# Kernel tuning notes

Hardware: AMD Instinct MI355X
Metric: run time of the kernel (lower is better)

Reference implementation:

```python
import jax, jax.numpy as jnp
import numpy as np
from jax import lax

K = 3        # kernel size
PAD = 1      # padding
K2 = K * K


def conv2d(x, w, b):
    # x: [B,C,H,W], w: [O,C,K,K], b: [O]
    y = lax.conv_general_dilated(
        x, w, window_strides=(1, 1), padding=((PAD, PAD), (PAD, PAD)),
        dimension_numbers=("NCHW", "OIHW", "NCHW"))
    return y + b[None, :, None, None]


def bilinear_sample(img, py, px):
    # img: [C,H,W]; py, px: [K2,H,W] float sampling coords (zero padding outside)
    H, W = img.shape[1], img.shape[2]
    y0 = jnp.floor(py); x0 = jnp.floor(px)
    wy1 = py - y0; wx1 = px - x0
    wy0 = 1.0 - wy1; wx0 = 1.0 - wx1

    def gather(yi, xi, wgt):
        yc = jnp.clip(yi, 0, H - 1).astype(jnp.int32)
        xc = jnp.clip(xi, 0, W - 1).astype(jnp.int32)
        valid = ((yi >= 0) & (yi <= H - 1) & (xi >= 0) & (xi <= W - 1))
        v = img[:, yc, xc]                      # [C,K2,H,W]
        return v * (wgt * valid.astype(img.dtype))[None]

    return (gather(y0, x0, wy0 * wx0) + gather(y0, x0 + 1, wy0 * wx1)
            + gather(y0 + 1, x0, wy1 * wx0) + gather(y0 + 1, x0 + 1, wy1 * wx1))


def deform_conv2d(x, offset, weight, bias):
    # x: [B,C,H,W], offset: [B,2*K2,H,W] as (dy,dx) pairs per kernel tap
    B, C, H, W = x.shape
    off = offset.reshape(B, K2, 2, H, W)
    ks_y = (jnp.arange(K2) // K - PAD).astype(x.dtype)   # kernel tap y offsets
    ks_x = (jnp.arange(K2) % K - PAD).astype(x.dtype)
    base_y = ks_y[:, None, None] + jnp.arange(H, dtype=x.dtype)[None, :, None]
    base_x = ks_x[:, None, None] + jnp.arange(W, dtype=x.dtype)[None, None, :]
    py = off[:, :, 0] + base_y                            # [B,K2,H,W]
    px = off[:, :, 1] + base_x
    sampled = jax.vmap(bilinear_sample)(x, py, px)        # [B,C,K2,H,W]
    out = jnp.einsum("bckhw,ock->bohw", sampled, weight.reshape(weight.shape[0], C, K2))
    return out + bias[None, :, None, None]


def setup_inputs() -> dict:
    key = jax.random.key(0)
    ks = jax.random.split(key, 5)
    B, C, O, H, W = 4, 64, 64, 128, 128
    s_off = 1.0 / np.sqrt(C * K2)
    return {
        "x": jax.random.normal(ks[0], (B, C, H, W), dtype=jnp.float32),
        "w_off": jax.random.normal(ks[1], (2 * K2, C, K, K), dtype=jnp.float32) * s_off,
        "b_off": jnp.zeros((2 * K2,), dtype=jnp.float32),
        "weight": jax.random.normal(ks[2], (O, C, K, K), dtype=jnp.float32) * s_off,
        "bias": jax.random.normal(ks[3], (O,), dtype=jnp.float32) * 0.01,
    }


def reference(x, w_off, b_off, weight, bias):
    offset = conv2d(x, w_off, b_off)          # [B,18,H,W]
    return deform_conv2d(x, offset, weight, bias)
```

## Files before the change

kernel.cpp:

```cpp
#include <hip/hip_runtime.h>
#include <hip/hip_bf16.h>

#define BB 4
#define CC 64
#define OO 64
#define HH 128
#define WW 128
#define HW (HH * WW)
#define K2 9
#define OCOFF 18
#define SMP_STRIDE 36

typedef __attribute__((ext_vector_type(8))) short short8;
typedef __attribute__((ext_vector_type(16))) float f32x16;

union U8 { unsigned u[4]; short8 s8; };

__device__ __forceinline__ float uf(unsigned u) { return __builtin_bit_cast(float, u); }

__device__ __forceinline__ unsigned cvtpk(float a, float b) {
  unsigned r;
  asm("v_cvt_pk_bf16_f32 %0, %1, %2" : "=v"(r) : "v"(a), "v"(b));
  return r;
}
__device__ __forceinline__ void split2(float a, float b, unsigned& ph, unsigned& pl) {
  ph = cvtpk(a, b);
  float ra = a - uf(ph << 16);
  float rb = b - uf(ph & 0xFFFF0000u);
  pl = cvtpk(ra, rb);
}

__device__ __forceinline__ unsigned short bf16_rne(float v) {
  unsigned u = __builtin_bit_cast(unsigned, v);
  return (unsigned short)((u + 0x7FFFu + ((u >> 16) & 1u)) >> 16);
}
__device__ __forceinline__ void bf16_split(float v, unsigned short& hi, unsigned short& lo) {
  hi = bf16_rne(v);
  float hf = __builtin_bit_cast(float, (unsigned)hi << 16);
  lo = bf16_rne(v - hf);
}
__device__ __forceinline__ float4 ld4(const float* p) { return *(const float4*)p; }

__global__ __launch_bounds__(256) void prep_all(
    const float* __restrict__ x, const float* __restrict__ weight,
    const float* __restrict__ w_off, float* __restrict__ xt,
    unsigned* __restrict__ wf, unsigned* __restrict__ wof) {
  int blk = blockIdx.x;
  int t = threadIdx.x;
  if (blk < 2048) {
    __shared__ float tile[64][33];
    int wt = blk & 3, h = (blk >> 2) & 127, b = blk >> 9;
    int w0 = wt * 32;
    {
      int w_l = t & 31, c_l = t >> 5;
#pragma unroll
      for (int i = 0; i < 8; ++i) {
        int cc = c_l * 8 + i;
        tile[cc][w_l] = x[(((size_t)b * 64 + cc) * 128 + h) * 128 + w0 + w_l];
      }
    }
    __syncthreads();
    {
      int c_w = t & 63, w_w = t >> 6;
#pragma unroll
      for (int i = 0; i < 8; ++i) {
        int wl = w_w * 8 + i;
        xt[(((size_t)b * 128 + h) * 128 + w0 + wl) * 64 + c_w] = tile[c_w][wl];
      }
    }
    return;
  }
  if (blk < 2048 + 144) {
    int d = (blk - 2048) * 256 + t;
    if (d >= 9 * 4096) return;
    int j2 = d & 3, l = (d >> 2) & 63, hh = (d >> 8) & 1, s = (d >> 9) & 3,
        m = (d >> 11) & 1, c = d >> 12;
    int o = m * 32 + (l & 31);
    int g = l >> 5;
    int ch0 = s * 16 + g * 8 + j2 * 2;
    float v0 = weight[(o * 64 + ch0) * 9 + c];
    float v1 = weight[(o * 64 + ch0 + 1) * 9 + c];
    unsigned short h0, l0, h1, l1;
    bf16_split(v0, h0, l0);
    bf16_split(v1, h1, l1);
    unsigned short b0 = hh ? l0 : h0;
    unsigned short b1 = hh ? l1 : h1;
    wf[d] = (unsigned)b0 | ((unsigned)b1 << 16);
    return;
  }
  {
    int d = (blk - 2192) * 256 + t;
    if (d >= 9 * 2048) return;
    int j2 = d & 3, l = (d >> 2) & 63, hh = (d >> 8) & 1, s = (d >> 9) & 3,
        c = d >> 11;
    int oc = l & 31;
    int g = l >> 5;
    int ch0 = s * 16 + g * 8 + j2 * 2;
    unsigned r = 0;
    if (oc < OCOFF) {
      float v0 = w_off[(oc * 64 + ch0) * 9 + c];
      float v1 = w_off[(oc * 64 + ch0 + 1) * 9 + c];
      unsigned short h0, l0, h1, l1;
      bf16_split(v0, h0, l0);
      bf16_split(v1, h1, l1);
      unsigned short b0 = hh ? l0 : h0;
      unsigned short b1 = hh ? l1 : h1;
      r = (unsigned)b0 | ((unsigned)b1 << 16);
    }
    wof[d] = r;
    return;
  }
}

struct TapD { int o00, o01, o10, o11; float w00, w01, w10, w11; };
struct TapW { float w00, w01, w10, w11; };

__device__ __forceinline__ TapD mk_tapd(float oyv, float oxv, int h, int wpix, int kk) {
  TapD t;
  const int dy = kk / 3 - 1, dx = kk - (kk / 3) * 3 - 1;
  float py = oyv + (float)(h + dy);
  float px = oxv + (float)(wpix + dx);
  float y0f = floorf(py), x0f = floorf(px);
  float wy1 = py - y0f, wx1 = px - x0f;
  float wy0 = 1.0f - wy1, wx0 = 1.0f - wx1;
  int y0 = (int)y0f, x0 = (int)x0f, y1 = y0 + 1, x1 = x0 + 1;
  bool vy0 = (unsigned)y0 < (unsigned)HH, vy1 = (unsigned)y1 < (unsigned)HH;
  bool vx0 = (unsigned)x0 < (unsigned)WW, vx1 = (unsigned)x1 < (unsigned)WW;
  t.w00 = (vy0 && vx0) ? wy0 * wx0 : 0.0f;
  t.w01 = (vy0 && vx1) ? wy0 * wx1 : 0.0f;
  t.w10 = (vy1 && vx0) ? wy1 * wx0 : 0.0f;
  t.w11 = (vy1 && vx1) ? wy1 * wx1 : 0.0f;
  int y0c = min(max(y0, 0), HH - 1), y1c = min(max(y1, 0), HH - 1);
  int x0c = min(max(x0, 0), WW - 1), x1c = min(max(x1, 0), WW - 1);
  t.o00 = (y0c * WW + x0c) * CC;
  t.o01 = (y0c * WW + x1c) * CC;
  t.o10 = (y1c * WW + x0c) * CC;
  t.o11 = (y1c * WW + x1c) * CC;
  return t;
}

__device__ __forceinline__ TapW stageD2(float4 (&st)[8], const float* xb,
                                        const float* ol, int h, int wbase,
                                        int pq, int j4, int r, int c) {
  float2 o = *(const float2*)&ol[(r * 8 + pq) * OCOFF + 2 * c];
  TapD t = mk_tapd(o.x, o.y, h, wbase + r * 8 + pq, c);
  st[0] = ld4(xb + t.o00 + j4);      st[1] = ld4(xb + t.o01 + j4);
  st[2] = ld4(xb + t.o10 + j4);      st[3] = ld4(xb + t.o11 + j4);
  st[4] = ld4(xb + t.o00 + 32 + j4); st[5] = ld4(xb + t.o01 + 32 + j4);
  st[6] = ld4(xb + t.o10 + 32 + j4); st[7] = ld4(xb + t.o11 + 32 + j4);
  TapW w = { t.w00, t.w01, t.w10, t.w11 };
  return w;
}

__device__ __forceinline__ void consD(unsigned* mh, unsigned* ml,
                                      int pl, int j,
                                      const float4 (&st)[8], const TapW& t) {
#pragma unroll
  for (int hf = 0; hf < 2; ++hf) {
    float v[4];
#pragma unroll
    for (int q = 0; q < 4; ++q)
      v[q] = fmaf(t.w00, st[hf * 4 + 0][q], fmaf(t.w01, st[hf * 4 + 1][q],
             fmaf(t.w10, st[hf * 4 + 2][q], t.w11 * st[hf * 4 + 3][q])));
    unsigned h01, l01, h23, l23;
    split2(v[0], v[1], h01, l01);
    split2(v[2], v[3], h23, l23);
    int idx = pl * SMP_STRIDE + hf * 16 + j * 2;
    *(uint2*)&mh[idx] = make_uint2(h01, h23);
    *(uint2*)&ml[idx] = make_uint2(l01, l23);
  }
}

__device__ __forceinline__ void p2_mfma(f32x16& acc0, f32x16& acc1,
                                        const unsigned* mh, const unsigned* ml,
                                        const unsigned* wfrag,
                                        int P, int g, int l, int c) {
  __builtin_amdgcn_s_setprio(1);
#pragma unroll
  for (int s = 0; s < 4; ++s) {
    int ridx = P * SMP_STRIDE + s * 8 + g * 4;
    short8 sh8 = *(const short8*)&mh[ridx];
    short8 sl8 = *(const short8*)&ml[ridx];
    const unsigned* wb = wfrag + ((size_t)((c * 16 + s * 2) * 64 + l)) * 4;
    short8 wh0 = *(const short8*)(wb);
    short8 wl0 = *(const short8*)(wb + 256);
    short8 wh1 = *(const short8*)(wb + 2048);
    short8 wl1 = *(const short8*)(wb + 2304);
    acc0 = __builtin_amdgcn_mfma_f32_32x32x16_bf16(wh0, sh8, acc0, 0, 0, 0);
    acc0 = __builtin_amdgcn_mfma_f32_32x32x16_bf16(wh0, sl8, acc0, 0, 0, 0);
    acc0 = __builtin_amdgcn_mfma_f32_32x32x16_bf16(wl0, sh8, acc0, 0, 0, 0);
    acc1 = __builtin_amdgcn_mfma_f32_32x32x16_bf16(wh1, sh8, acc1, 0, 0, 0);
    acc1 = __builtin_amdgcn_mfma_f32_32x32x16_bf16(wh1, sl8, acc1, 0, 0, 0);
    acc1 = __builtin_amdgcn_mfma_f32_32x32x16_bf16(wl1, sh8, acc1, 0, 0, 0);
  }
  __builtin_amdgcn_s_setprio(0);
}

__device__ __forceinline__ unsigned stageO1(uint4 (&T)[8], const float* xb,
                                            int h, int wP, int g, int c) {
  const int dy = c / 3 - 1, dx = c - (c / 3) * 3 - 1;
  const int y = h + dy, xp = wP + dx;
  bool valid = ((unsigned)y < (unsigned)HH) && ((unsigned)xp < (unsigned)WW);
  int yc = min(max(y, 0), HH - 1), xc = min(max(xp, 0), WW - 1);
  const uint4* rowp = (const uint4*)(xb + (size_t)(yc * WW + xc) * CC);
#pragma unroll
  for (int s = 0; s < 4; ++s) {
    T[2 * s]     = rowp[s * 4 + g * 2];
    T[2 * s + 1] = rowp[s * 4 + g * 2 + 1];
  }
  return valid ? 0xFFFFFFFFu : 0u;
}

__device__ __forceinline__ void p1_tap(f32x16& accO, uint4 (&TC)[8], unsigned mskC,
                                       uint4 (&TN)[8], unsigned& mskN,
                                       const float* xb, const unsigned* wofrag,
                                       int h, int wP, int g, int l, int c, bool last) {
  if (!last) {
    mskN = stageO1(TN, xb, h, wP, g, c + 1);
    __builtin_amdgcn_sched_barrier(0);
  }
#pragma unroll
  for (int s = 0; s < 4; ++s) {
    uint4 u0 = TC[2 * s], u1 = TC[2 * s + 1];
    u0.x &= mskC; u0.y &= mskC; u0.z &= mskC; u0.w &= mskC;
    u1.x &= mskC; u1.y &= mskC; u1.z &= mskC; u1.w &= mskC;
    U8 sh, sl;
    split2(uf(u0.x), uf(u0.y), sh.u[0], sl.u[0]);
    split2(uf(u0.z), uf(u0.w), sh.u[1], sl.u[1]);
    split2(uf(u1.x), uf(u1.y), sh.u[2], sl.u[2]);
    split2(uf(u1.z), uf(u1.w), sh.u[3], sl.u[3]);
    const unsigned* wb = wofrag + ((size_t)((c * 8 + s * 2) * 64 + l)) * 4;
    short8 wh = *(const short8*)(wb);
    short8 wl = *(const short8*)(wb + 256);
    __builtin_amdgcn_s_setprio(1);
    accO = __builtin_amdgcn_mfma_f32_32x32x16_bf16(wh, sh.s8, accO, 0, 0, 0);
    accO = __builtin_amdgcn_mfma_f32_32x32x16_bf16(wh, sl.s8, accO, 0, 0, 0);
    accO = __builtin_amdgcn_mfma_f32_32x32x16_bf16(wl, sh.s8, accO, 0, 0, 0);
    __builtin_amdgcn_s_setprio(0);
  }
}

__device__ __forceinline__ void p2_tap(
    f32x16& acc0, f32x16& acc1,
    float4 (&S0)[8], float4 (&S1)[8], float4 (&S2)[8], float4 (&S3)[8],
    TapW& t0, TapW& t1, TapW& t2, TapW& t3,
    unsigned* mh, unsigned* ml, const float* xb, const float* ol,
    const unsigned* wfrag, int h, int wbase, int pq, int j, int j4,
    int P, int g, int l, int c, bool last) {
  t2 = stageD2(S2, xb, ol, h, wbase, pq, j4, 2, c);
  __builtin_amdgcn_sched_barrier(0);
  consD(mh, ml, 0 * 8 + pq, j, S0, t0);
  t3 = stageD2(S3, xb, ol, h, wbase, pq, j4, 3, c);
  __builtin_amdgcn_sched_barrier(0);
  consD(mh, ml, 1 * 8 + pq, j, S1, t1);
  if (!last) {
    t0 = stageD2(S0, xb, ol, h, wbase, pq, j4, 0, c + 1);
    __builtin_amdgcn_sched_barrier(0);
  }
  consD(mh, ml, 2 * 8 + pq, j, S2, t2);
  if (!last) {
    t1 = stageD2(S1, xb, ol, h, wbase, pq, j4, 1, c + 1);
    __builtin_amdgcn_sched_barrier(0);
  }
  consD(mh, ml, 3 * 8 + pq, j, S3, t3);
  p2_mfma(acc0, acc1, mh, ml, wfrag, P, g, l, c);
}

__global__ __launch_bounds__(128, 2) void fused_deform(
    const float* __restrict__ xt, const unsigned* __restrict__ wfrag,
    const unsigned* __restrict__ wofrag, const float* __restrict__ b_off,
    const float* __restrict__ bias, float* __restrict__ out) {
  __shared__ __align__(16) unsigned smph[2][32 * SMP_STRIDE];
  __shared__ __align__(16) unsigned smpl[2][32 * SMP_STRIDE];
  __shared__ __align__(16) float offs_lds[2][32 * OCOFF];

  const int blk = blockIdx.x;
  const int sx = (blk & 7) * 128 + (blk >> 3);
  const int seg = sx & 1, h = (sx >> 1) & 127, b = sx >> 8;
  const int tid = threadIdx.x;
  const int l = tid & 63, wv = tid >> 6;
  const int P = l & 31, g = l >> 5;
  const int j = l & 7, pq = l >> 3;
  const int j4 = j * 4;
  const int wbase = seg * 64 + wv * 32;

  const float* xb = xt + (size_t)b * HW * CC;
  unsigned* mh = smph[wv];
  unsigned* ml = smpl[wv];
  float* ol = offs_lds[wv];

  {
    f32x16 accO = {0,0,0,0,0,0,0,0,0,0,0,0,0,0,0,0};
    uint4 TA[8], TB[8];
    unsigned mskA = 0, mskB = 0;
    mskA = stageO1(TA, xb, h, wbase + P, g, 0);
    __builtin_amdgcn_sched_barrier(0);
    p1_tap(accO, TA, mskA, TB, mskB, xb, wofrag, h, wbase + P, g, l, 0, false);
    p1_tap(accO, TB, mskB, TA, mskA, xb, wofrag, h, wbase + P, g, l, 1, false);
    p1_tap(accO, TA, mskA, TB, mskB, xb, wofrag, h, wbase + P, g, l, 2, false);
    p1_tap(accO, TB, mskB, TA, mskA, xb, wofrag, h, wbase + P, g, l, 3, false);
    p1_tap(accO, TA, mskA, TB, mskB, xb, wofrag, h, wbase + P, g, l, 4, false);
    p1_tap(accO, TB, mskB, TA, mskA, xb, wofrag, h, wbase + P, g, l, 5, false);
    p1_tap(accO, TA, mskA, TB, mskB, xb, wofrag, h, wbase + P, g, l, 6, false);
    p1_tap(accO, TB, mskB, TA, mskA, xb, wofrag, h, wbase + P, g, l, 7, false);
    p1_tap(accO, TA, mskA, TB, mskB, xb, wofrag, h, wbase + P, g, l, 8, true);
#pragma unroll
    for (int r = 0; r < 16; ++r) {
      int oc = (r & 3) + 8 * (r >> 2) + 4 * g;
      if (oc < OCOFF) ol[P * OCOFF + oc] = accO[r] + b_off[oc];
    }
  }

  f32x16 acc0 = {0,0,0,0,0,0,0,0,0,0,0,0,0,0,0,0};
  f32x16 acc1 = {0,0,0,0,0,0,0,0,0,0,0,0,0,0,0,0};
  {
    float4 S0[8], S1[8], S2[8], S3[8];
    TapW t0, t1, t2, t3;
    t0 = stageD2(S0, xb, ol, h, wbase, pq, j4, 0, 0);
    __builtin_amdgcn_sched_barrier(0);
    t1 = stageD2(S1, xb, ol, h, wbase, pq, j4, 1, 0);
    __builtin_amdgcn_sched_barrier(0);
    p2_tap(acc0, acc1, S0, S1, S2, S3, t0, t1, t2, t3, mh, ml, xb, ol, wfrag,
           h, wbase, pq, j, j4, P, g, l, 0, false);
    p2_tap(acc0, acc1, S0, S1, S2, S3, t0, t1, t2, t3, mh, ml, xb, ol, wfrag,
           h, wbase, pq, j, j4, P, g, l, 1, false);
    p2_tap(acc0, acc1, S0, S1, S2, S3, t0, t1, t2, t3, mh, ml, xb, ol, wfrag,
           h, wbase, pq, j, j4, P, g, l, 2, false);
    p2_tap(acc0, acc1, S0, S1, S2, S3, t0, t1, t2, t3, mh, ml, xb, ol, wfrag,
           h, wbase, pq, j, j4, P, g, l, 3, false);
    p2_tap(acc0, acc1, S0, S1, S2, S3, t0, t1, t2, t3, mh, ml, xb, ol, wfrag,
           h, wbase, pq, j, j4, P, g, l, 4, false);
    p2_tap(acc0, acc1, S0, S1, S2, S3, t0, t1, t2, t3, mh, ml, xb, ol, wfrag,
           h, wbase, pq, j, j4, P, g, l, 5, false);
    p2_tap(acc0, acc1, S0, S1, S2, S3, t0, t1, t2, t3, mh, ml, xb, ol, wfrag,
           h, wbase, pq, j, j4, P, g, l, 6, false);
    p2_tap(acc0, acc1, S0, S1, S2, S3, t0, t1, t2, t3, mh, ml, xb, ol, wfrag,
           h, wbase, pq, j, j4, P, g, l, 7, false);
    p2_tap(acc0, acc1, S0, S1, S2, S3, t0, t1, t2, t3, mh, ml, xb, ol, wfrag,
           h, wbase, pq, j, j4, P, g, l, 8, true);
  }

  const int wpix = wbase + P;
#pragma unroll
  for (int r = 0; r < 16; ++r) {
    int o0 = (r & 3) + 8 * (r >> 2) + 4 * g;
    out[(((size_t)b * 64 + o0) * 128 + h) * 128 + wpix] = acc0[r] + bias[o0];
    out[(((size_t)b * 64 + 32 + o0) * 128 + h) * 128 + wpix] = acc1[r] + bias[32 + o0];
  }
}

extern "C" void kernel_launch(void* const* d_in, const int* in_sizes, int n_in,
                              void* d_out, int out_size, void* d_ws, size_t ws_size,
                              hipStream_t stream) {
  const float* x      = (const float*)d_in[0];
  const float* w_off  = (const float*)d_in[1];
  const float* b_off  = (const float*)d_in[2];
  const float* weight = (const float*)d_in[3];
  const float* bias   = (const float*)d_in[4];
  float* out = (float*)d_out;

  float*    xt     = (float*)d_ws;
  unsigned* wfrag  = (unsigned*)(xt + (size_t)4194304);
  unsigned* wofrag = wfrag + 36864;

  prep_all<<<2264, 256, 0, stream>>>(x, weight, w_off, xt, wfrag, wofrag);
  fused_deform<<<1024, 128, 0, stream>>>(xt, wfrag, wofrag, b_off, bias, out);
}
```

Measured before the change: 136.1 us.

## Split channel reduction across two extra waves with LDS cross-wave reduction

Doubles the block to 256 threads by splitting the 64 input channels of both the offset conv and the deform GEMM across two wave halves. Partial accumulators are combined through a new LDS reduction buffer, and the offset results are shared block-wide. Per-wave register staging is halved (three 4-entry stage buffers instead of four 8-entry ones), which is meant to raise occupancy and latency hiding. The cost is extra __syncthreads, LDS traffic for the reductions, and half the waves sitting idle during output stores.

```diff
diff --git a/kernel.cpp b/kernel.cpp
--- a/kernel.cpp
+++ b/kernel.cpp
@@ -9,7 +9,7 @@
 #define HW (HH * WW)
 #define K2 9
 #define OCOFF 18
-#define SMP_STRIDE 36
+#define STRD 20
 
 typedef __attribute__((ext_vector_type(8))) short short8;
 typedef __attribute__((ext_vector_type(16))) float f32x16;
@@ -139,48 +139,90 @@
   return t;
 }
 
-__device__ __forceinline__ TapW stageD2(float4 (&st)[8], const float* xb,
-                                        const float* ol, int h, int wbase,
-                                        int pq, int j4, int r, int c) {
-  float2 o = *(const float2*)&ol[(r * 8 + pq) * OCOFF + 2 * c];
+__device__ __forceinline__ unsigned stageO1K(uint4 (&T)[4], const float* xb,
+                                             int h, int wP, int chb, int g, int c) {
+  const int dy = c / 3 - 1, dx = c - (c / 3) * 3 - 1;
+  const int y = h + dy, xp = wP + dx;
+  bool valid = ((unsigned)y < (unsigned)HH) && ((unsigned)xp < (unsigned)WW);
+  int yc = min(max(y, 0), HH - 1), xc = min(max(xp, 0), WW - 1);
+  const uint4* rowp = (const uint4*)(xb + (size_t)(yc * WW + xc) * CC);
+#pragma unroll
+  for (int si = 0; si < 2; ++si) {
+    int u4i = (chb + si * 16 + g * 8) >> 2;
+    T[2 * si]     = rowp[u4i];
+    T[2 * si + 1] = rowp[u4i + 1];
+  }
+  return valid ? 0xFFFFFFFFu : 0u;
+}
+
+__device__ __forceinline__ void p1_tapK(f32x16& accO, uint4 (&TC)[4], unsigned mskC,
+                                        uint4 (&TN)[4], unsigned& mskN,
+                                        const float* xb, const unsigned* wofrag,
+                                        int h, int wP, int chb, int g, int l,
+                                        int sh, int c, bool last) {
+  if (!last) {
+    mskN = stageO1K(TN, xb, h, wP, chb, g, c + 1);
+    __builtin_amdgcn_sched_barrier(0);
+  }
+#pragma unroll
+  for (int si = 0; si < 2; ++si) {
+    uint4 u0 = TC[2 * si], u1 = TC[2 * si + 1];
+    u0.x &= mskC; u0.y &= mskC; u0.z &= mskC; u0.w &= mskC;
+    u1.x &= mskC; u1.y &= mskC; u1.z &= mskC; u1.w &= mskC;
+    U8 sv, lv;
+    split2(uf(u0.x), uf(u0.y), sv.u[0], lv.u[0]);
+    split2(uf(u0.z), uf(u0.w), sv.u[1], lv.u[1]);
+    split2(uf(u1.x), uf(u1.y), sv.u[2], lv.u[2]);
+    split2(uf(u1.z), uf(u1.w), sv.u[3], lv.u[3]);
+    const int s = sh * 2 + si;
+    const unsigned* wb = wofrag + ((size_t)((c * 8 + s * 2) * 64 + l)) * 4;
+    short8 wh = *(const short8*)(wb);
+    short8 wl = *(const short8*)(wb + 256);
+    __builtin_amdgcn_s_setprio(1);
+    accO = __builtin_amdgcn_mfma_f32_32x32x16_bf16(wh, sv.s8, accO, 0, 0, 0);
+    accO = __builtin_amdgcn_mfma_f32_32x32x16_bf16(wh, lv.s8, accO, 0, 0, 0);
+    accO = __builtin_amdgcn_mfma_f32_32x32x16_bf16(wl, sv.s8, accO, 0, 0, 0);
+    __builtin_amdgcn_s_setprio(0);
+  }
+}
+
+__device__ __forceinline__ TapW stageD2K(float4 (&st)[4], const float* xb,
+                                         const float* ol, int h, int wbase,
+                                         int pgl0, int pq, int chj, int r, int c) {
+  float2 o = *(const float2*)&ol[(pgl0 + r * 8 + pq) * OCOFF + 2 * c];
   TapD t = mk_tapd(o.x, o.y, h, wbase + r * 8 + pq, c);
-  st[0] = ld4(xb + t.o00 + j4);      st[1] = ld4(xb + t.o01 + j4);
-  st[2] = ld4(xb + t.o10 + j4);      st[3] = ld4(xb + t.o11 + j4);
-  st[4] = ld4(xb + t.o00 + 32 + j4); st[5] = ld4(xb + t.o01 + 32 + j4);
-  st[6] = ld4(xb + t.o10 + 32 + j4); st[7] = ld4(xb + t.o11 + 32 + j4);
+  st[0] = ld4(xb + t.o00 + chj);  st[1] = ld4(xb + t.o01 + chj);
+  st[2] = ld4(xb + t.o10 + chj);  st[3] = ld4(xb + t.o11 + chj);
   TapW w = { t.w00, t.w01, t.w10, t.w11 };
   return w;
 }
 
-__device__ __forceinline__ void consD(unsigned* mh, unsigned* ml,
-                                      int pl, int j,
-                                      const float4 (&st)[8], const TapW& t) {
-#pragma unroll
-  for (int hf = 0; hf < 2; ++hf) {
-    float v[4];
-#pragma unroll
-    for (int q = 0; q < 4; ++q)
-      v[q] = fmaf(t.w00, st[hf * 4 + 0][q], fmaf(t.w01, st[hf * 4 + 1][q],
-             fmaf(t.w10, st[hf * 4 + 2][q], t.w11 * st[hf * 4 + 3][q])));
-    unsigned h01, l01, h23, l23;
-    split2(v[0], v[1], h01, l01);
-    split2(v[2], v[3], h23, l23);
-    int idx = pl * SMP_STRIDE + hf * 16 + j * 2;
-    *(uint2*)&mh[idx] = make_uint2(h01, h23);
-    *(uint2*)&ml[idx] = make_uint2(l01, l23);
-  }
-}
-
-__device__ __forceinline__ void p2_mfma(f32x16& acc0, f32x16& acc1,
-                                        const unsigned* mh, const unsigned* ml,
-                                        const unsigned* wfrag,
-                                        int P, int g, int l, int c) {
+__device__ __forceinline__ void consDK(unsigned* mh, unsigned* ml, int pl, int j,
+                                       const float4 (&st)[4], const TapW& t) {
+  float v[4];
+#pragma unroll
+  for (int q = 0; q < 4; ++q)
+    v[q] = fmaf(t.w00, st[0][q], fmaf(t.w01, st[1][q],
+           fmaf(t.w10, st[2][q], t.w11 * st[3][q])));
+  unsigned h01, l01, h23, l23;
+  split2(v[0], v[1], h01, l01);
+  split2(v[2], v[3], h23, l23);
+  int idx = pl * STRD + j * 2;
+  *(uint2*)&mh[idx] = make_uint2(h01, h23);
+  *(uint2*)&ml[idx] = make_uint2(l01, l23);
+}
+
+__device__ __forceinline__ void p2_mfmaK(f32x16& acc0, f32x16& acc1,
+                                         const unsigned* mh, const unsigned* ml,
+                                         const unsigned* wfrag,
+                                         int P, int g, int l, int sh, int c) {
   __builtin_amdgcn_s_setprio(1);
 #pragma unroll
-  for (int s = 0; s < 4; ++s) {
-    int ridx = P * SMP_STRIDE + s * 8 + g * 4;
+  for (int si = 0; si < 2; ++si) {
+    int ridx = P * STRD + si * 8 + g * 4;
     short8 sh8 = *(const short8*)&mh[ridx];
     short8 sl8 = *(const short8*)&ml[ridx];
+    const int s = sh * 2 + si;
     const unsigned* wb = wfrag + ((size_t)((c * 16 + s * 2) * 64 + l)) * 4;
     short8 wh0 = *(const short8*)(wb);
     short8 wl0 = *(const short8*)(wb + 256);
@@ -196,156 +238,145 @@
   __builtin_amdgcn_s_setprio(0);
 }
 
-__device__ __forceinline__ unsigned stageO1(uint4 (&T)[8], const float* xb,
-                                            int h, int wP, int g, int c) {
-  const int dy = c / 3 - 1, dx = c - (c / 3) * 3 - 1;
-  const int y = h + dy, xp = wP + dx;
-  bool valid = ((unsigned)y < (unsigned)HH) && ((unsigned)xp < (unsigned)WW);
-  int yc = min(max(y, 0), HH - 1), xc = min(max(xp, 0), WW - 1);
-  const uint4* rowp = (const uint4*)(xb + (size_t)(yc * WW + xc) * CC);
-#pragma unroll
-  for (int s = 0; s < 4; ++s) {
-    T[2 * s]     = rowp[s * 4 + g * 2];
-    T[2 * s + 1] = rowp[s * 4 + g * 2 + 1];
-  }
-  return valid ? 0xFFFFFFFFu : 0u;
-}
-
-__device__ __forceinline__ void p1_tap(f32x16& accO, uint4 (&TC)[8], unsigned mskC,
-                                       uint4 (&TN)[8], unsigned& mskN,
-                                       const float* xb, const unsigned* wofrag,
-                                       int h, int wP, int g, int l, int c, bool last) {
+__device__ __forceinline__ void p2_tapK(f32x16& acc0, f32x16& acc1,
+    float4 (&SA)[4], float4 (&SB)[4], float4 (&SC)[4],
+    TapW& tA, TapW& tB, TapW& tC,
+    unsigned* mh, unsigned* ml, const float* xb, const float* ol,
+    const unsigned* wfrag, int h, int wbase, int pgl0, int pq, int j, int chj,
+    int P, int g, int l, int sh, int c, bool last) {
+  tC = stageD2K(SC, xb, ol, h, wbase, pgl0, pq, chj, 2, c);
+  __builtin_amdgcn_sched_barrier(0);
+  consDK(mh, ml, 0 * 8 + pq, j, SA, tA);
+  tA = stageD2K(SA, xb, ol, h, wbase, pgl0, pq, chj, 3, c);
+  __builtin_amdgcn_sched_barrier(0);
+  consDK(mh, ml, 1 * 8 + pq, j, SB, tB);
   if (!last) {
-    mskN = stageO1(TN, xb, h, wP, g, c + 1);
-    __builtin_amdgcn_sched_barrier(0);
-  }
-#pragma unroll
-  for (int s = 0; s < 4; ++s) {
-    uint4 u0 = TC[2 * s], u1 = TC[2 * s + 1];
-    u0.x &= mskC; u0.y &= mskC; u0.z &= mskC; u0.w &= mskC;
-    u1.x &= mskC; u1.y &= mskC; u1.z &= mskC; u1.w &= mskC;
-    U8 sh, sl;
-    split2(uf(u0.x), uf(u0.y), sh.u[0], sl.u[0]);
-    split2(uf(u0.z), uf(u0.w), sh.u[1], sl.u[1]);
-    split2(uf(u1.x), uf(u1.y), sh.u[2], sl.u[2]);
-    split2(uf(u1.z), uf(u1.w), sh.u[3], sl.u[3]);
-    const unsigned* wb = wofrag + ((size_t)((c * 8 + s * 2) * 64 + l)) * 4;
-    short8 wh = *(const short8*)(wb);
-    short8 wl = *(const short8*)(wb + 256);
-    __builtin_amdgcn_s_setprio(1);
-    accO = __builtin_amdgcn_mfma_f32_32x32x16_bf16(wh, sh.s8, accO, 0, 0, 0);
-    accO = __builtin_amdgcn_mfma_f32_32x32x16_bf16(wh, sl.s8, accO, 0, 0, 0);
-    accO = __builtin_amdgcn_mfma_f32_32x32x16_bf16(wl, sh.s8, accO, 0, 0, 0);
-    __builtin_amdgcn_s_setprio(0);
-  }
-}
-
-__device__ __forceinline__ void p2_tap(
-    f32x16& acc0, f32x16& acc1,
-    float4 (&S0)[8], float4 (&S1)[8], float4 (&S2)[8], float4 (&S3)[8],
-    TapW& t0, TapW& t1, TapW& t2, TapW& t3,
-    unsigned* mh, unsigned* ml, const float* xb, const float* ol,
-    const unsigned* wfrag, int h, int wbase, int pq, int j, int j4,
-    int P, int g, int l, int c, bool last) {
-  t2 = stageD2(S2, xb, ol, h, wbase, pq, j4, 2, c);
-  __builtin_amdgcn_sched_barrier(0);
-  consD(mh, ml, 0 * 8 + pq, j, S0, t0);
-  t3 = stageD2(S3, xb, ol, h, wbase, pq, j4, 3, c);
-  __builtin_amdgcn_sched_barrier(0);
-  consD(mh, ml, 1 * 8 + pq, j, S1, t1);
+    tB = stageD2K(SB, xb, ol, h, wbase, pgl0, pq, chj, 0, c + 1);
+    __builtin_amdgcn_sched_barrier(0);
+  }
+  consDK(mh, ml, 2 * 8 + pq, j, SC, tC);
   if (!last) {
-    t0 = stageD2(S0, xb, ol, h, wbase, pq, j4, 0, c + 1);
-    __builtin_amdgcn_sched_barrier(0);
-  }
-  consD(mh, ml, 2 * 8 + pq, j, S2, t2);
-  if (!last) {
-    t1 = stageD2(S1, xb, ol, h, wbase, pq, j4, 1, c + 1);
-    __builtin_amdgcn_sched_barrier(0);
-  }
-  consD(mh, ml, 3 * 8 + pq, j, S3, t3);
-  p2_mfma(acc0, acc1, mh, ml, wfrag, P, g, l, c);
-}
-
-__global__ __launch_bounds__(128, 2) void fused_deform(
+    tC = stageD2K(SC, xb, ol, h, wbase, pgl0, pq, chj, 1, c + 1);
+    __builtin_amdgcn_sched_barrier(0);
+  }
+  consDK(mh, ml, 3 * 8 + pq, j, SA, tA);
+  p2_mfmaK(acc0, acc1, mh, ml, wfrag, P, g, l, sh, c);
+}
+
+__global__ __launch_bounds__(256, 4) void fused_deform(
     const float* __restrict__ xt, const unsigned* __restrict__ wfrag,
     const unsigned* __restrict__ wofrag, const float* __restrict__ b_off,
     const float* __restrict__ bias, float* __restrict__ out) {
-  __shared__ __align__(16) unsigned smph[2][32 * SMP_STRIDE];
-  __shared__ __align__(16) unsigned smpl[2][32 * SMP_STRIDE];
-  __shared__ __align__(16) float offs_lds[2][32 * OCOFF];
+  __shared__ __align__(16) unsigned smph[4][32 * STRD];
+  __shared__ __align__(16) unsigned smpl[4][32 * STRD];
+  __shared__ __align__(16) float ol[64 * OCOFF];
+  __shared__ __align__(16) float lred[2][64][17];
 
   const int blk = blockIdx.x;
   const int sx = (blk & 7) * 128 + (blk >> 3);
   const int seg = sx & 1, h = (sx >> 1) & 127, b = sx >> 8;
   const int tid = threadIdx.x;
   const int l = tid & 63, wv = tid >> 6;
+  const int pg = wv & 1, sh = wv >> 1;
   const int P = l & 31, g = l >> 5;
   const int j = l & 7, pq = l >> 3;
-  const int j4 = j * 4;
-  const int wbase = seg * 64 + wv * 32;
+  const int wbase = seg * 64 + pg * 32;
+  const int pgl0 = pg * 32;
+  const int chb = sh * 32;
+  const int chj = chb + j * 4;
 
   const float* xb = xt + (size_t)b * HW * CC;
   unsigned* mh = smph[wv];
   unsigned* ml = smpl[wv];
-  float* ol = offs_lds[wv];
 
   {
     f32x16 accO = {0,0,0,0,0,0,0,0,0,0,0,0,0,0,0,0};
-    uint4 TA[8], TB[8];
+    const int wP = wbase + P;
+    uint4 TA[4], TB[4];
     unsigned mskA = 0, mskB = 0;
-    mskA = stageO1(TA, xb, h, wbase + P, g, 0);
-    __builtin_amdgcn_sched_barrier(0);
-    p1_tap(accO, TA, mskA, TB, mskB, xb, wofrag, h, wbase + P, g, l, 0, false);
-    p1_tap(accO, TB, mskB, TA, mskA, xb, wofrag, h, wbase + P, g, l, 1, false);
-    p1_tap(accO, TA, mskA, TB, mskB, xb, wofrag, h, wbase + P, g, l, 2, false);
-    p1_tap(accO, TB, mskB, TA, mskA, xb, wofrag, h, wbase + P, g, l, 3, false);
-    p1_tap(accO, TA, mskA, TB, mskB, xb, wofrag, h, wbase + P, g, l, 4, false);
-    p1_tap(accO, TB, mskB, TA, mskA, xb, wofrag, h, wbase + P, g, l, 5, false);
-    p1_tap(accO, TA, mskA, TB, mskB, xb, wofrag, h, wbase + P, g, l, 6, false);
-    p1_tap(accO, TB, mskB, TA, mskA, xb, wofrag, h, wbase + P, g, l, 7, false);
-    p1_tap(accO, TA, mskA, TB, mskB, xb, wofrag, h, wbase + P, g, l, 8, true);
-#pragma unroll
-    for (int r = 0; r < 16; ++r) {
-      int oc = (r & 3) + 8 * (r >> 2) + 4 * g;
-      if (oc < OCOFF) ol[P * OCOFF + oc] = accO[r] + b_off[oc];
-    }
+    mskA = stageO1K(TA, xb, h, wP, chb, g, 0);
+    __builtin_amdgcn_sched_barrier(0);
+    p1_tapK(accO, TA, mskA, TB, mskB, xb, wofrag, h, wP, chb, g, l, sh, 0, false);
+    p1_tapK(accO, TB, mskB, TA, mskA, xb, wofrag, h, wP, chb, g, l, sh, 1, false);
+    p1_tapK(accO, TA, mskA, TB, mskB, xb, wofrag, h, wP, chb, g, l, sh, 2, false);
+    p1_tapK(accO, TB, mskB, TA, mskA, xb, wofrag, h, wP, chb, g, l, sh, 3, false);
+    p1_tapK(accO, TA, mskA, TB, mskB, xb, wofrag, h, wP, chb, g, l, sh, 4, false);
+    p1_tapK(accO, TB, mskB, TA, mskA, xb, wofrag, h, wP, chb, g, l, sh, 5, false);
+    p1_tapK(accO, TA, mskA, TB, mskB, xb, wofrag, h, wP, chb, g, l, sh, 6, false);
+    p1_tapK(accO, TB, mskB, TA, mskA, xb, wofrag, h, wP, chb, g, l, sh, 7, false);
+    p1_tapK(accO, TA, mskA, TB, mskB, xb, wofrag, h, wP, chb, g, l, sh, 8, true);
+    if (sh == 1) {
+#pragma unroll
+      for (int r = 0; r < 16; ++r) lred[pg][l][r] = accO[r];
+    }
+    __syncthreads();
+    if (sh == 0) {
+#pragma unroll
+      for (int r = 0; r < 16; ++r) {
+        int oc = (r & 3) + 8 * (r >> 2) + 4 * g;
+        if (oc < OCOFF)
+          ol[(pgl0 + P) * OCOFF + oc] = accO[r] + lred[pg][l][r] + b_off[oc];
+      }
+    }
+    __syncthreads();
   }
 
   f32x16 acc0 = {0,0,0,0,0,0,0,0,0,0,0,0,0,0,0,0};
   f32x16 acc1 = {0,0,0,0,0,0,0,0,0,0,0,0,0,0,0,0};
   {
-    float4 S0[8], S1[8], S2[8], S3[8];
-    TapW t0, t1, t2, t3;
-    t0 = stageD2(S0, xb, ol, h, wbase, pq, j4, 0, 0);
-    __builtin_amdgcn_sched_barrier(0);
-    t1 = stageD2(S1, xb, ol, h, wbase, pq, j4, 1, 0);
-    __builtin_amdgcn_sched_barrier(0);
-    p2_tap(acc0, acc1, S0, S1, S2, S3, t0, t1, t2, t3, mh, ml, xb, ol, wfrag,
-           h, wbase, pq, j, j4, P, g, l, 0, false);
-    p2_tap(acc0, acc1, S0, S1, S2, S3, t0, t1, t2, t3, mh, ml, xb, ol, wfrag,
-           h, wbase, pq, j, j4, P, g, l, 1, false);
-    p2_tap(acc0, acc1, S0, S1, S2, S3, t0, t1, t2, t3, mh, ml, xb, ol, wfrag,
-           h, wbase, pq, j, j4, P, g, l, 2, false);
-    p2_tap(acc0, acc1, S0, S1, S2, S3, t0, t1, t2, t3, mh, ml, xb, ol, wfrag,
-           h, wbase, pq, j, j4, P, g, l, 3, false);
-    p2_tap(acc0, acc1, S0, S1, S2, S3, t0, t1, t2, t3, mh, ml, xb, ol, wfrag,
-           h, wbase, pq, j, j4, P, g, l, 4, false);
-    p2_tap(acc0, acc1, S0, S1, S2, S3, t0, t1, t2, t3, mh, ml, xb, ol, wfrag,
-           h, wbase, pq, j, j4, P, g, l, 5, false);
-    p2_tap(acc0, acc1, S0, S1, S2, S3, t0, t1, t2, t3, mh, ml, xb, ol, wfrag,
-           h, wbase, pq, j, j4, P, g, l, 6, false);
-    p2_tap(acc0, acc1, S0, S1, S2, S3, t0, t1, t2, t3, mh, ml, xb, ol, wfrag,
-           h, wbase, pq, j, j4, P, g, l, 7, false);
-    p2_tap(acc0, acc1, S0, S1, S2, S3, t0, t1, t2, t3, mh, ml, xb, ol, wfrag,
-           h, wbase, pq, j, j4, P, g, l, 8, true);
+    float4 S0[4], S1[4], S2[4];
+    TapW t0, t1, t2;
+    t0 = stageD2K(S0, xb, ol, h, wbase, pgl0, pq, chj, 0, 0);
+    __builtin_amdgcn_sched_barrier(0);
+    t1 = stageD2K(S1, xb, ol, h, wbase, pgl0, pq, chj, 1, 0);
+    __builtin_amdgcn_sched_barrier(0);
+    p2_tapK(acc0, acc1, S0, S1, S2, t0, t1, t2, mh, ml, xb, ol, wfrag,
+            h, wbase, pgl0, pq, j, chj, P, g, l, sh, 0, false);
+    p2_tapK(acc0, acc1, S1, S2, S0, t1, t2, t0, mh, ml, xb, ol, wfrag,
+            h, wbase, pgl0, pq, j, chj, P, g, l, sh, 1, false);
+    p2_tapK(acc0, acc1, S2, S0, S1, t2, t0, t1, mh, ml, xb, ol, wfrag,
+            h, wbase, pgl0, pq, j, chj, P, g, l, sh, 2, false);
+    p2_tapK(acc0, acc1, S0, S1, S2, t0, t1, t2, mh, ml, xb, ol, wfrag,
+            h, wbase, pgl0, pq, j, chj, P, g, l, sh, 3, false);
+    p2_tapK(acc0, acc1, S1, S2, S0, t1, t2, t0, mh, ml, xb, ol, wfrag,
+            h, wbase, pgl0, pq, j, chj, P, g, l, sh, 4, false);
+    p2_tapK(acc0, acc1, S2, S0, S1, t2, t0, t1, mh, ml, xb, ol, wfrag,
+            h, wbase, pgl0, pq, j, chj, P, g, l, sh, 5, false);
+    p2_tapK(acc0, acc1, S0, S1, S2, t0, t1, t2, mh, ml, xb, ol, wfrag,
+            h, wbase, pgl0, pq, j, chj, P, g, l, sh, 6, false);
+    p2_tapK(acc0, acc1, S1, S2, S0, t1, t2, t0, mh, ml, xb, ol, wfrag,
+            h, wbase, pgl0, pq, j, chj, P, g, l, sh, 7, false);
+    p2_tapK(acc0, acc1, S2, S0, S1, t2, t0, t1, mh, ml, xb, ol, wfrag,
+            h, wbase, pgl0, pq, j, chj, P, g, l, sh, 8, true);
   }
 
   const int wpix = wbase + P;
-#pragma unroll
-  for (int r = 0; r < 16; ++r) {
-    int o0 = (r & 3) + 8 * (r >> 2) + 4 * g;
-    out[(((size_t)b * 64 + o0) * 128 + h) * 128 + wpix] = acc0[r] + bias[o0];
-    out[(((size_t)b * 64 + 32 + o0) * 128 + h) * 128 + wpix] = acc1[r] + bias[32 + o0];
+  if (sh == 1) {
+#pragma unroll
+    for (int r = 0; r < 16; ++r) lred[pg][l][r] = acc0[r];
+  }
+  __syncthreads();
+  if (sh == 0) {
+#pragma unroll
+    for (int r = 0; r < 16; ++r) {
+      int o0 = (r & 3) + 8 * (r >> 2) + 4 * g;
+      out[(((size_t)b * 64 + o0) * 128 + h) * 128 + wpix] =
+          acc0[r] + lred[pg][l][r] + bias[o0];
+    }
+  }
+  __syncthreads();
+  if (sh == 1) {
+#pragma unroll
+    for (int r = 0; r < 16; ++r) lred[pg][l][r] = acc1[r];
+  }
+  __syncthreads();
+  if (sh == 0) {
+#pragma unroll
+    for (int r = 0; r < 16; ++r) {
+      int o0 = (r & 3) + 8 * (r >> 2) + 4 * g;
+      out[(((size_t)b * 64 + 32 + o0) * 128 + h) * 128 + wpix] =
+          acc1[r] + lred[pg][l][r] + bias[32 + o0];
+    }
   }
 }
 
@@ -364,5 +395,5 @@
   unsigned* wofrag = wfrag + 36864;
 
   prep_all<<<2264, 256, 0, stream>>>(x, weight, w_off, xt, wfrag, wofrag);
-  fused_deform<<<1024, 128, 0, stream>>>(xt, wfrag, wofrag, b_off, bias, out);
-}
+  fused_deform<<<1024, 256, 0, stream>>>(xt, wfrag, wofrag, b_off, bias, out);
+}
```

Result: no change. 138.6 us (+1.9%).
